# Kernel optimization log

Hardware: AMD Instinct MI355X
Metric: run time of the kernel (lower is better)

Reference implementation:

```python
import jax, jax.numpy as jnp
import numpy as np

NUM_GRAPHS = 10  # seq_len graphs batched together


def _gat_layer(x, W, al, ar, b, src, dst, n_nodes):
    # x: [N, h_dim]; W: [h_dim, H*D]; al/ar/b: [H, D]
    H, D = al.shape
    feat = (x @ W).reshape(-1, H, D)                      # [N, H, D]
    el = jnp.einsum('nhd,hd->nh', feat, al)               # [N, H]
    er = jnp.einsum('nhd,hd->nh', feat, ar)               # [N, H]
    e = jax.nn.leaky_relu(el[src] + er[dst], 0.2)         # [E, H]
    # edge softmax over incoming edges of each dst node (stable)
    emax = jax.ops.segment_max(e, dst, num_segments=n_nodes)
    emax = jnp.where(jnp.isfinite(emax), emax, 0.0)
    w = jnp.exp(e - emax[dst])                            # [E, H]
    denom = jax.ops.segment_sum(w, dst, num_segments=n_nodes)  # [N, H]
    msg = w[:, :, None] * feat[src]                       # [E, H, D]
    agg = jax.ops.segment_sum(msg, dst, num_segments=n_nodes)  # [N, H, D]
    out = agg / jnp.maximum(denom, 1e-9)[:, :, None] + b
    return out.mean(axis=1)                               # [N, h_dim] (mean over heads)


def setup_inputs() -> dict:
    key = jax.random.key(0)
    ks = jax.random.split(key, 16)
    N, E, V, h, H = 100000, 1000000, 50000, 64, 3
    node_ids = jax.random.randint(ks[0], (N,), 0, V)
    edge_src = jax.random.randint(ks[1], (E,), 0, N)
    edge_dst = jax.random.randint(ks[2], (E,), 0, N)
    node_graph_id = jnp.sort(jax.random.randint(ks[3], (N,), 0, NUM_GRAPHS))
    s = 1.0 / np.sqrt(h)
    return {
        'node_ids': node_ids, 'edge_src': edge_src, 'edge_dst': edge_dst,
        'node_graph_id': node_graph_id,
        'W_embed': jax.random.normal(ks[4], (V, h), jnp.float32),
        'W1': jax.random.normal(ks[5], (h, H * h), jnp.float32) * s,
        'al1': jax.random.normal(ks[6], (H, h), jnp.float32) * s,
        'ar1': jax.random.normal(ks[7], (H, h), jnp.float32) * s,
        'b1': jnp.zeros((H, h), jnp.float32),
        'W2': jax.random.normal(ks[8], (h, H * h), jnp.float32) * s,
        'al2': jax.random.normal(ks[9], (H, h), jnp.float32) * s,
        'ar2': jax.random.normal(ks[10], (H, h), jnp.float32) * s,
        'b2': jnp.zeros((H, h), jnp.float32),
    }


def reference(node_ids, edge_src, edge_dst, node_graph_id, W_embed,
              W1, al1, ar1, b1, W2, al2, ar2, b2):
    n_nodes = node_ids.shape[0]
    h = W_embed[node_ids]                                 # gather embeddings
    h = _gat_layer(h, W1, al1, ar1, b1, edge_src, edge_dst, n_nodes)
    h = _gat_layer(h, W2, al2, ar2, b2, edge_src, edge_dst, n_nodes)
    # dgl.max_nodes: per-graph max pooling over nodes
    global_info = jax.ops.segment_max(h, node_graph_id, num_segments=NUM_GRAPHS)
    return global_info                                    # [NUM_GRAPHS, h_dim]
```

## Files before the change

### kernel.cpp

```cpp
#include <hip/hip_runtime.h>
#include <math.h>


#define HEADS 3
#define HD 64
#define FDIM (HEADS*HD)
#define NCOL 208
#define NUM_GRAPHS 10
#define NPB 32
#define FROWB 384

typedef short bf16x8 __attribute__((ext_vector_type(8)));
typedef float f32x4  __attribute__((ext_vector_type(4)));

__device__ __forceinline__ float bf2f(unsigned short u) {
    return __uint_as_float(((unsigned int)u) << 16);
}
__device__ __forceinline__ unsigned short f2bf(float f) {
    unsigned int u = __float_as_uint(f);
    unsigned int r = (u + 0x7FFFu + ((u >> 16) & 1u)) >> 16;
    return (unsigned short)r;
}

__device__ __forceinline__ int wave_incl_scan(int v, int lane) {
#pragma unroll
    for (int off = 1; off < 64; off <<= 1) {
        int t = __shfl_up(v, off);
        if (lane >= off) v += t;
    }
    return v;
}

__device__ __forceinline__ unsigned int fmap(float f) {
    unsigned int u = __float_as_uint(f);
    return (u & 0x80000000u) ? ~u : (u | 0x80000000u);
}
__device__ __forceinline__ float funmap(unsigned int u) {
    u = (u & 0x80000000u) ? (u & 0x7FFFFFFFu) : ~u;
    return __uint_as_float(u);
}

__global__ void k_prep(const float* __restrict__ W1, const float* __restrict__ al1,
                       const float* __restrict__ ar1,
                       const float* __restrict__ W2, const float* __restrict__ al2,
                       const float* __restrict__ ar2,
                       unsigned short* __restrict__ Wt1, unsigned short* __restrict__ Wt2,
                       unsigned int* __restrict__ gm) {
    int i = blockIdx.x * blockDim.x + threadIdx.x;
    if (i < 2 * NCOL * HD) {
        int l = i / (NCOL * HD), j = i % (NCOL * HD);
        int c = j >> 6, k = j & 63;
        const float* W  = l ? W2  : W1;
        const float* al = l ? al2 : al1;
        const float* ar = l ? ar2 : ar1;
        unsigned short* Wt = l ? Wt2 : Wt1;
        float v = 0.f;
        if (c < FDIM) {
            v = W[k * FDIM + c];
        } else if (c < FDIM + 6) {
            int h = c - FDIM;
            const float* a = (h < 3) ? al : ar;
            int hh = (h < 3) ? h : h - 3;
            float s = 0.f;
            for (int d = 0; d < HD; ++d)
                s += W[k * FDIM + hh * HD + d] * a[hh * HD + d];
            v = s;
        }
        Wt[j] = f2bf(v);
    }
    if (i < NUM_GRAPHS * HD) gm[i] = 0x007FFFFFu;
}

__global__ void k_hist(const int* __restrict__ dst, int* __restrict__ deg, int E) {
    int i = blockIdx.x * blockDim.x + threadIdx.x;
    if (i < E) atomicAdd(&deg[dst[i]], 1);
}

__global__ void k_scan1(const int* __restrict__ deg, int* __restrict__ tmp,
                        int* __restrict__ partials, int N) {
    int t = threadIdx.x, b = blockIdx.x;
    int i = b * 256 + t;
    int v = (i < N) ? deg[i] : 0;
    int lane = t & 63, w = t >> 6;
    int incl = wave_incl_scan(v, lane);
    __shared__ int wsum[4];
    if (lane == 63) wsum[w] = incl;
    __syncthreads();
    int off = 0;
    for (int j = 0; j < w; ++j) off += wsum[j];
    incl += off;
    if (i < N) tmp[i] = incl;
    if (t == 255) partials[b] = incl;
}

__global__ void k_scan2(int* __restrict__ partials, int nb) {
    int t = threadIdx.x;
    int v = (t < nb) ? partials[t] : 0;
    int lane = t & 63, w = t >> 6;
    int incl = wave_incl_scan(v, lane);
    __shared__ int wsum[8];
    if (lane == 63) wsum[w] = incl;
    __syncthreads();
    int off = 0;
    for (int j = 0; j < w; ++j) off += wsum[j];
    incl += off;
    if (t < nb) partials[t] = incl;
}

__global__ void k_scan3(const int* __restrict__ tmp, const int* __restrict__ deg,
                        const int* __restrict__ partials, int* __restrict__ rowptr,
                        int* __restrict__ cur, int N) {
    int i = blockIdx.x * blockDim.x + threadIdx.x;
    if (i >= N) return;
    int b = i >> 8;
    int off = b ? partials[b - 1] : 0;
    int incl = tmp[i] + off;
    rowptr[i + 1] = incl;
    cur[i] = incl - deg[i];
    if (i == 0) rowptr[0] = 0;
}

__device__ __forceinline__ void feat_body(
        const unsigned short* __restrict__ xbf, const int* __restrict__ ids,
        const float* __restrict__ Wemb, const unsigned short* __restrict__ Wt,
        unsigned char* __restrict__ featB, float4* __restrict__ el4,
        float4* __restrict__ er4, int N, int blk) {
    __shared__ unsigned short xs[NPB][72];
    __shared__ unsigned short ls[NPB][200];
    int t = threadIdx.x;
    int lane = t & 63, w = t >> 6;
    int base = blk * NPB;

    if (ids) {
        for (int i = t; i < NPB * 16; i += 256) {
            int row = i >> 4, c4 = (i & 15) * 4;
            int n = base + row;
            float4 v = {0.f, 0.f, 0.f, 0.f};
            if (n < N) v = *(const float4*)(Wemb + (size_t)ids[n] * HD + c4);
            unsigned short* dp = &xs[row][c4];
            dp[0] = f2bf(v.x); dp[1] = f2bf(v.y); dp[2] = f2bf(v.z); dp[3] = f2bf(v.w);
        }
    } else {
        for (int i = t; i < NPB * 16; i += 256) {
            int row = i >> 4, c4 = (i & 15) * 4;
            int n = base + row;
            ushort4 v = {0, 0, 0, 0};
            if (n < N) v = *(const ushort4*)(xbf + (size_t)n * HD + c4);
            *(ushort4*)(&xs[row][c4]) = v;
        }
    }

    int ntile = (w == 3) ? 4 : 3;
    bf16x8 bfrag[4][2];
#pragma unroll
    for (int c = 0; c < 4; ++c) {
        if (c >= ntile) break;
#pragma unroll
        for (int kk = 0; kk < 2; ++kk) {
            int coln = (w * 3 + c) * 16 + (lane & 15);
            int k0 = kk * 32 + (lane >> 4) * 8;
            bfrag[c][kk] = *(const bf16x8*)(Wt + (size_t)coln * HD + k0);
        }
    }
    __syncthreads();

    f32x4 acc[2][4];
#pragma unroll
    for (int r = 0; r < 2; ++r)
#pragma unroll
        for (int c = 0; c < 4; ++c) acc[r][c] = (f32x4){0.f, 0.f, 0.f, 0.f};
#pragma unroll
    for (int r = 0; r < 2; ++r)
#pragma unroll
        for (int kk = 0; kk < 2; ++kk) {
            int row = r * 16 + (lane & 15);
            int k0 = kk * 32 + (lane >> 4) * 8;
            bf16x8 a = *(const bf16x8*)(&xs[row][k0]);
#pragma unroll
            for (int c = 0; c < 4; ++c) {
                if (c >= ntile) break;
                acc[r][c] = __builtin_amdgcn_mfma_f32_16x16x32_bf16(a, bfrag[c][kk], acc[r][c], 0, 0, 0);
            }
        }

#pragma unroll
    for (int r = 0; r < 2; ++r)
#pragma unroll
        for (int c = 0; c < 3; ++c) {
            int col = (w * 3 + c) * 16 + (lane & 15);
#pragma unroll
            for (int j = 0; j < 4; ++j) {
                int row = r * 16 + (lane >> 4) * 4 + j;
                ls[row][col] = f2bf(acc[r][c][j]);
            }
        }

    if (w == 3) {
        int col = lane & 15;
        if (col < 6) {
#pragma unroll
            for (int r = 0; r < 2; ++r)
#pragma unroll
                for (int j = 0; j < 4; ++j) {
                    int row = r * 16 + (lane >> 4) * 4 + j;
                    int n = base + row;
                    if (n < N) {
                        float v = acc[r][3][j];
                        if (col < 3) ((float*)&el4[n])[col] = v;
                        else         ((float*)&er4[n])[col - 3] = v;
                    }
                }
        }
    }
    __syncthreads();

    for (int i = t; i < NPB * 64; i += 256) {
        int row = i >> 6, d = i & 63;
        int n = base + row;
        if (n < N) {
            unsigned int u = ((unsigned int)ls[row][64 + d] << 16) | (unsigned int)ls[row][d];
            *(unsigned int*)(featB + (size_t)n * FROWB + d * 4) = u;
        }
    }
    for (int i = t; i < NPB * 32; i += 256) {
        int row = i >> 5, dd = (i & 31) * 2;
        int n = base + row;
        if (n < N) {
            unsigned int u = (unsigned int)ls[row][128 + dd] |
                             ((unsigned int)ls[row][128 + dd + 1] << 16);
            *(unsigned int*)(featB + (size_t)n * FROWB + 256 + dd * 2) = u;
        }
    }
}

__global__ __launch_bounds__(256) void k_feat_mfma(
        const unsigned short* __restrict__ xbf, const int* __restrict__ ids,
        const float* __restrict__ Wemb, const unsigned short* __restrict__ Wt,
        unsigned char* __restrict__ featB, float4* __restrict__ el4,
        float4* __restrict__ er4, int N) {
    feat_body(xbf, ids, Wemb, Wt, featB, el4, er4, N, blockIdx.x);
}

__global__ __launch_bounds__(256) void k_feat1_scatter(
        const int* __restrict__ ids, const float* __restrict__ Wemb,
        const unsigned short* __restrict__ Wt,
        unsigned char* __restrict__ featB, float4* __restrict__ el4,
        float4* __restrict__ er4, int N,
        const int* __restrict__ src, const int* __restrict__ dst,
        int* __restrict__ cur, int* __restrict__ csrc, int E) {
    int g = blockIdx.x / 9, r = blockIdx.x % 9;
    if (r < 4) {
        int fb = g * 4 + r;
        if (fb * NPB < N)
            feat_body(nullptr, ids, Wemb, Wt, featB, el4, er4, N, fb);
    } else {
        int sb = g * 5 + (r - 4);
        int i = sb * 256 + (int)threadIdx.x;
        if (i < E) {
            int pos = atomicAdd(&cur[dst[i]], 1);
            csrc[pos] = src[i];
        }
    }
}

__global__ void k_gather(const int* __restrict__ rowptr, const int* __restrict__ csrc,
                         const float4* __restrict__ el4, const float4* __restrict__ er4,
                         const unsigned char* __restrict__ featB,
                         const float* __restrict__ b,
                         unsigned short* __restrict__ xout, int N) {
    __shared__ float4 stage[4][64];
    int wid = (blockIdx.x * blockDim.x + threadIdx.x) >> 6;
    int lane = threadIdx.x & 63, w = (threadIdx.x >> 6) & 3;
    if (wid >= N) return;
    int beg = rowptr[wid], end = rowptr[wid + 1];
    int deg = end - beg;
    float4 er = er4[wid];
    float acc0 = 0.f, acc1 = 0.f, acc2 = 0.f;
    float ds0 = 0.f, ds1 = 0.f, ds2 = 0.f;
    for (int cb = 0; cb < deg; cb += 64) {
        int nch = min(64, deg - cb);
        if (lane < nch) {
            int s = csrc[beg + cb + lane];
            float4 l = el4[s];
            float e0 = l.x + er.x; e0 = e0 >= 0.f ? e0 : 0.2f * e0;
            float e1 = l.y + er.y; e1 = e1 >= 0.f ? e1 : 0.2f * e1;
            float e2 = l.z + er.z; e2 = e2 >= 0.f ? e2 : 0.2f * e2;
            float4 o;
            o.x = __int_as_float(s);
            o.y = __expf(e0); o.z = __expf(e1); o.w = __expf(e2);
            stage[w][lane] = o;
        }
        __builtin_amdgcn_wave_barrier();
#pragma unroll 4
        for (int j = 0; j < nch; ++j) {
            float4 e = stage[w][j];
            int s = __float_as_int(e.x);
            const unsigned char* frow = featB + (size_t)s * FROWB;
            unsigned int u01 = *(const unsigned int*)(frow + (size_t)lane * 4);
            unsigned short h2 = *(const unsigned short*)(frow + 256 + (size_t)lane * 2);
            float f0 = __uint_as_float(u01 << 16);
            float f1 = __uint_as_float(u01 & 0xffff0000u);
            acc0 = fmaf(e.y, f0, acc0);
            acc1 = fmaf(e.z, f1, acc1);
            acc2 = fmaf(e.w, bf2f(h2), acc2);
            ds0 += e.y; ds1 += e.z; ds2 += e.w;
        }
        __builtin_amdgcn_wave_barrier();
    }
    float o = (acc0 / fmaxf(ds0, 1e-9f) + b[lane])
            + (acc1 / fmaxf(ds1, 1e-9f) + b[HD + lane])
            + (acc2 / fmaxf(ds2, 1e-9f) + b[2 * HD + lane]);
    xout[(size_t)wid * HD + lane] = f2bf(o * (1.f / 3.f));
}

__global__ void k_gmax(const unsigned short* __restrict__ x, const int* __restrict__ gid,
                       unsigned int* __restrict__ gm, int N) {
    int lane = threadIdx.x;
    int base = blockIdx.x * 64;
    int endn = min(base + 64, N);
    int cur = -1;
    float m = 0.f;
    for (int n = base; n < endn; ++n) {
        int g = gid[n];
        float v = bf2f(x[(size_t)n * HD + lane]);
        if (g != cur) {
            if (cur >= 0) atomicMax(&gm[cur * HD + lane], fmap(m));
            cur = g; m = v;
        } else {
            m = fmaxf(m, v);
        }
    }
    if (cur >= 0) atomicMax(&gm[cur * HD + lane], fmap(m));
}

__global__ void k_gmax_final(const unsigned int* __restrict__ gm, float* __restrict__ out) {
    int i = blockIdx.x * blockDim.x + threadIdx.x;
    if (i < NUM_GRAPHS * HD) out[i] = funmap(gm[i]);
}

extern "C" void kernel_launch(void* const* d_in, const int* in_sizes, int n_in,
                              void* d_out, int out_size, void* d_ws, size_t ws_size,
                              hipStream_t stream) {
    const int*   node_ids = (const int*)d_in[0];
    const int*   edge_src = (const int*)d_in[1];
    const int*   edge_dst = (const int*)d_in[2];
    const int*   gid      = (const int*)d_in[3];
    const float* Wemb     = (const float*)d_in[4];
    const float* W1  = (const float*)d_in[5];
    const float* al1 = (const float*)d_in[6];
    const float* ar1 = (const float*)d_in[7];
    const float* b1  = (const float*)d_in[8];
    const float* W2  = (const float*)d_in[9];
    const float* al2 = (const float*)d_in[10];
    const float* ar2 = (const float*)d_in[11];
    const float* b2  = (const float*)d_in[12];

    int N = in_sizes[0];
    int E = in_sizes[1];

    char* p = (char*)d_ws;
    auto alloc = [&](size_t bytes) {
        char* r = p;
        p += (bytes + 255) & ~(size_t)255;
        return (void*)r;
    };
    int*   deg      = (int*)alloc((size_t)N * 4);
    int*   tmp      = (int*)alloc((size_t)N * 4);
    int*   partials = (int*)alloc(512 * 4);
    int*   rowptr   = (int*)alloc((size_t)(N + 1) * 4);
    int*   cur      = (int*)alloc((size_t)N * 4);
    int*   csrc     = (int*)alloc((size_t)E * 4);
    unsigned char* featB = (unsigned char*)alloc((size_t)N * FROWB);
    unsigned short* Wt1  = (unsigned short*)alloc((size_t)NCOL * HD * 2);
    unsigned short* Wt2  = (unsigned short*)alloc((size_t)NCOL * HD * 2);
    float4* el4     = (float4*)alloc((size_t)N * 16);
    float4* er4     = (float4*)alloc((size_t)N * 16);
    unsigned short* x1b = (unsigned short*)alloc((size_t)N * HD * 2);
    unsigned int* gm = (unsigned int*)alloc(NUM_GRAPHS * HD * 4);
    (void)ws_size;

    int nb = (N + 255) / 256;

    hipMemsetAsync(deg, 0, (size_t)N * 4, stream);
    k_prep<<<dim3((2 * NCOL * HD + 255) / 256), dim3(256), 0, stream>>>(
        W1, al1, ar1, W2, al2, ar2, Wt1, Wt2, gm);
    k_hist<<<dim3((E + 255) / 256), dim3(256), 0, stream>>>(edge_dst, deg, E);
    k_scan1<<<dim3(nb), dim3(256), 0, stream>>>(deg, tmp, partials, N);
    k_scan2<<<dim3(1), dim3(512), 0, stream>>>(partials, nb);
    k_scan3<<<dim3(nb), dim3(256), 0, stream>>>(tmp, deg, partials, rowptr, cur, N);

    dim3 featGrid((N + NPB - 1) / NPB), featBlk(256);
    dim3 aggGrid((N * 64 + 255) / 256), aggBlk(256);

    int nf = (N + NPB - 1) / NPB;
    int ns = (E + 255) / 256;
    int ngroups = ((nf + 3) / 4 > (ns + 4) / 5) ? (nf + 3) / 4 : (ns + 4) / 5;
    dim3 fusedGrid(ngroups * 9);

    k_feat1_scatter<<<fusedGrid, featBlk, 0, stream>>>(
        node_ids, Wemb, Wt1, featB, el4, er4, N,
        edge_src, edge_dst, cur, csrc, E);
    k_gather<<<aggGrid, aggBlk, 0, stream>>>(rowptr, csrc, el4, er4, featB, b1, x1b, N);

    k_feat_mfma<<<featGrid, featBlk, 0, stream>>>(x1b, nullptr, nullptr, Wt2,
                                                  featB, el4, er4, N);
    k_gather<<<aggGrid, aggBlk, 0, stream>>>(rowptr, csrc, el4, er4, featB, b2, x1b, N);

    k_gmax<<<dim3((N + 63) / 64), dim3(64), 0, stream>>>(x1b, gid, gm, N);
    k_gmax_final<<<dim3(1), dim3(NUM_GRAPHS * HD), 0, stream>>>(gm, (float*)d_out);
}
```

Baseline: 302.3 us.

## Build CSR via two-level bucketed scatter and fuse prep with histogram

Replaces the per-node atomic scatter into CSR with a two-pass scheme: edges are first scattered into 64-node buckets via global atomics on bucket cursors, storing (src,dst) pairs, then a new kernel per bucket places them using shared-memory atomics. This aims to improve locality of the random-address atomics and writes. It also fuses weight prep with the degree histogram into one launch to save a launch. It adds an extra kernel, an 8-byte staging buffer and an extra pass over the edges, and bucket-cursor atomics contend more heavily.

```diff
diff --git a/kernel.cpp b/kernel.cpp
--- a/kernel.cpp
+++ b/kernel.cpp
@@ -9,6 +9,8 @@
 #define NUM_GRAPHS 10
 #define NPB 32
 #define FROWB 384
+#define BSH 6
+#define PREPB 104
 
 typedef short bf16x8 __attribute__((ext_vector_type(8)));
 typedef float f32x4  __attribute__((ext_vector_type(4)));
@@ -40,40 +42,41 @@
     return __uint_as_float(u);
 }
 
-__global__ void k_prep(const float* __restrict__ W1, const float* __restrict__ al1,
-                       const float* __restrict__ ar1,
-                       const float* __restrict__ W2, const float* __restrict__ al2,
-                       const float* __restrict__ ar2,
-                       unsigned short* __restrict__ Wt1, unsigned short* __restrict__ Wt2,
-                       unsigned int* __restrict__ gm) {
-    int i = blockIdx.x * blockDim.x + threadIdx.x;
-    if (i < 2 * NCOL * HD) {
-        int l = i / (NCOL * HD), j = i % (NCOL * HD);
-        int c = j >> 6, k = j & 63;
-        const float* W  = l ? W2  : W1;
-        const float* al = l ? al2 : al1;
-        const float* ar = l ? ar2 : ar1;
-        unsigned short* Wt = l ? Wt2 : Wt1;
-        float v = 0.f;
-        if (c < FDIM) {
-            v = W[k * FDIM + c];
-        } else if (c < FDIM + 6) {
-            int h = c - FDIM;
-            const float* a = (h < 3) ? al : ar;
-            int hh = (h < 3) ? h : h - 3;
-            float s = 0.f;
-            for (int d = 0; d < HD; ++d)
-                s += W[k * FDIM + hh * HD + d] * a[hh * HD + d];
-            v = s;
-        }
-        Wt[j] = f2bf(v);
-    }
-    if (i < NUM_GRAPHS * HD) gm[i] = 0x007FFFFFu;
-}
-
-__global__ void k_hist(const int* __restrict__ dst, int* __restrict__ deg, int E) {
-    int i = blockIdx.x * blockDim.x + threadIdx.x;
-    if (i < E) atomicAdd(&deg[dst[i]], 1);
+__global__ void k_prep_hist(const float* __restrict__ W1, const float* __restrict__ al1,
+                            const float* __restrict__ ar1,
+                            const float* __restrict__ W2, const float* __restrict__ al2,
+                            const float* __restrict__ ar2,
+                            unsigned short* __restrict__ Wt1, unsigned short* __restrict__ Wt2,
+                            unsigned int* __restrict__ gm,
+                            const int* __restrict__ dst, int* __restrict__ deg, int E) {
+    if (blockIdx.x < PREPB) {
+        int i = blockIdx.x * blockDim.x + threadIdx.x;
+        if (i < 2 * NCOL * HD) {
+            int l = i / (NCOL * HD), j = i % (NCOL * HD);
+            int c = j >> 6, k = j & 63;
+            const float* W  = l ? W2  : W1;
+            const float* al = l ? al2 : al1;
+            const float* ar = l ? ar2 : ar1;
+            unsigned short* Wt = l ? Wt2 : Wt1;
+            float v = 0.f;
+            if (c < FDIM) {
+                v = W[k * FDIM + c];
+            } else if (c < FDIM + 6) {
+                int h = c - FDIM;
+                const float* a = (h < 3) ? al : ar;
+                int hh = (h < 3) ? h : h - 3;
+                float s = 0.f;
+                for (int d = 0; d < HD; ++d)
+                    s += W[k * FDIM + hh * HD + d] * a[hh * HD + d];
+                v = s;
+            }
+            Wt[j] = f2bf(v);
+        }
+        if (i < NUM_GRAPHS * HD) gm[i] = 0x007FFFFFu;
+    } else {
+        int i = (blockIdx.x - PREPB) * blockDim.x + threadIdx.x;
+        if (i < E) atomicAdd(&deg[dst[i]], 1);
+    }
 }
 
 __global__ void k_scan1(const int* __restrict__ deg, int* __restrict__ tmp,
@@ -109,14 +112,15 @@
 
 __global__ void k_scan3(const int* __restrict__ tmp, const int* __restrict__ deg,
                         const int* __restrict__ partials, int* __restrict__ rowptr,
-                        int* __restrict__ cur, int N) {
+                        int* __restrict__ bcur, int N) {
     int i = blockIdx.x * blockDim.x + threadIdx.x;
     if (i >= N) return;
     int b = i >> 8;
     int off = b ? partials[b - 1] : 0;
     int incl = tmp[i] + off;
     rowptr[i + 1] = incl;
-    cur[i] = incl - deg[i];
+    int start = incl - deg[i];
+    if ((i & 63) == 0) bcur[i >> BSH] = start;
     if (i == 0) rowptr[0] = 0;
 }
 
@@ -247,7 +251,7 @@
         unsigned char* __restrict__ featB, float4* __restrict__ el4,
         float4* __restrict__ er4, int N,
         const int* __restrict__ src, const int* __restrict__ dst,
-        int* __restrict__ cur, int* __restrict__ csrc, int E) {
+        int* __restrict__ bcur, int2* __restrict__ staged, int E) {
     int g = blockIdx.x / 9, r = blockIdx.x % 9;
     if (r < 4) {
         int fb = g * 4 + r;
@@ -257,9 +261,29 @@
         int sb = g * 5 + (r - 4);
         int i = sb * 256 + (int)threadIdx.x;
         if (i < E) {
-            int pos = atomicAdd(&cur[dst[i]], 1);
-            csrc[pos] = src[i];
-        }
+            int s = src[i], d = dst[i];
+            int pos = atomicAdd(&bcur[d >> BSH], 1);
+            staged[pos] = make_int2(s, d);
+        }
+    }
+}
+
+__global__ __launch_bounds__(256) void k_scatter_fine(
+        const int* __restrict__ rowptr, const int2* __restrict__ staged,
+        int* __restrict__ csrc, int N) {
+    __shared__ int lcur[64];
+    int b = blockIdx.x;
+    int node0 = b << BSH;
+    int t = threadIdx.x;
+    int nn = N - node0; if (nn > 64) nn = 64;
+    if (t < nn) lcur[t] = rowptr[node0 + t];
+    __syncthreads();
+    int bstart = rowptr[node0];
+    int bend = rowptr[node0 + nn];
+    for (int i = bstart + t; i < bend; i += 256) {
+        int2 e = staged[i];
+        int pos = atomicAdd(&lcur[e.y - node0], 1);
+        csrc[pos] = e.x;
     }
 }
 
@@ -357,6 +381,7 @@
 
     int N = in_sizes[0];
     int E = in_sizes[1];
+    int NBK = (N + 63) >> BSH;
 
     char* p = (char*)d_ws;
     auto alloc = [&](size_t bytes) {
@@ -368,7 +393,8 @@
     int*   tmp      = (int*)alloc((size_t)N * 4);
     int*   partials = (int*)alloc(512 * 4);
     int*   rowptr   = (int*)alloc((size_t)(N + 1) * 4);
-    int*   cur      = (int*)alloc((size_t)N * 4);
+    int*   bcur     = (int*)alloc((size_t)NBK * 4);
+    int2*  staged   = (int2*)alloc((size_t)E * 8);
     int*   csrc     = (int*)alloc((size_t)E * 4);
     unsigned char* featB = (unsigned char*)alloc((size_t)N * FROWB);
     unsigned short* Wt1  = (unsigned short*)alloc((size_t)NCOL * HD * 2);
@@ -382,12 +408,11 @@
     int nb = (N + 255) / 256;
 
     hipMemsetAsync(deg, 0, (size_t)N * 4, stream);
-    k_prep<<<dim3((2 * NCOL * HD + 255) / 256), dim3(256), 0, stream>>>(
-        W1, al1, ar1, W2, al2, ar2, Wt1, Wt2, gm);
-    k_hist<<<dim3((E + 255) / 256), dim3(256), 0, stream>>>(edge_dst, deg, E);
+    k_prep_hist<<<dim3(PREPB + (E + 255) / 256), dim3(256), 0, stream>>>(
+        W1, al1, ar1, W2, al2, ar2, Wt1, Wt2, gm, edge_dst, deg, E);
     k_scan1<<<dim3(nb), dim3(256), 0, stream>>>(deg, tmp, partials, N);
     k_scan2<<<dim3(1), dim3(512), 0, stream>>>(partials, nb);
-    k_scan3<<<dim3(nb), dim3(256), 0, stream>>>(tmp, deg, partials, rowptr, cur, N);
+    k_scan3<<<dim3(nb), dim3(256), 0, stream>>>(tmp, deg, partials, rowptr, bcur, N);
 
     dim3 featGrid((N + NPB - 1) / NPB), featBlk(256);
     dim3 aggGrid((N * 64 + 255) / 256), aggBlk(256);
@@ -399,7 +424,8 @@
 
     k_feat1_scatter<<<fusedGrid, featBlk, 0, stream>>>(
         node_ids, Wemb, Wt1, featB, el4, er4, N,
-        edge_src, edge_dst, cur, csrc, E);
+        edge_src, edge_dst, bcur, staged, E);
+    k_scatter_fine<<<dim3(NBK), dim3(256), 0, stream>>>(rowptr, staged, csrc, N);
     k_gather<<<aggGrid, aggBlk, 0, stream>>>(rowptr, csrc, el4, er4, featB, b1, x1b, N);
 
     k_feat_mfma<<<featGrid, featBlk, 0, stream>>>(x1b, nullptr, nullptr, Wt2,
```

Measured after the change: 394.0 us. 30.3% more time.
